# Performance work log

Hardware: AMD Instinct MI355X
Metric: run time of the kernel (lower is better)

Reference implementation:

```python
import jax, jax.numpy as jnp
import numpy as np

D = 1024
H = 16
L = 2048
B = 2
EPS = 1e-5


def setup_inputs() -> dict:
    key = jax.random.key(0)
    ks = jax.random.split(key, 12)
    s = 0.02
    return {
        "x": jax.random.normal(ks[0], (B, L, D), dtype=jnp.float32),
        "ln1_w": jnp.ones((D,), jnp.float32),
        "ln1_b": jnp.zeros((D,), jnp.float32),
        "ln2_w": jnp.ones((D,), jnp.float32),
        "ln2_b": jnp.zeros((D,), jnp.float32),
        "attn_w": jax.random.normal(ks[1], (D, 3 * D), jnp.float32) * s,
        "attn_b": jnp.zeros((3 * D,), jnp.float32),
        "proj_w": jax.random.normal(ks[2], (D, D), jnp.float32) * s,
        "proj_b": jnp.zeros((D,), jnp.float32),
        "fc1_w": jax.random.normal(ks[3], (D, 4 * D), jnp.float32) * s,
        "fc1_b": jnp.zeros((4 * D,), jnp.float32),
        "fc2_w": jax.random.normal(ks[4], (4 * D, D), jnp.float32) * s,
        "fc2_b": jnp.zeros((D,), jnp.float32),
    }


def layernorm(x, w, b):
    mu = jnp.mean(x, axis=-1, keepdims=True)
    var = jnp.mean(jnp.square(x - mu), axis=-1, keepdims=True)
    return (x - mu) * jax.lax.rsqrt(var + EPS) * w + b


def reference(x, ln1_w, ln1_b, ln2_w, ln2_b, attn_w, attn_b,
              proj_w, proj_b, fc1_w, fc1_b, fc2_w, fc2_b):
    Bsz, Lq, C = x.shape
    hd = C // H

    # --- attention branch ---
    h = layernorm(x, ln1_w, ln1_b)
    qkv = h @ attn_w + attn_b                      # [B, L, 3C]
    q, k, v = jnp.split(qkv, 3, axis=-1)
    q = q.reshape(Bsz, Lq, H, hd).transpose(0, 2, 1, 3)  # [B, H, L, hd]
    k = k.reshape(Bsz, Lq, H, hd).transpose(0, 2, 1, 3)
    v = v.reshape(Bsz, Lq, H, hd).transpose(0, 2, 1, 3)

    # NOTE: original scales by 1/sqrt(embedding_dim), not sqrt(head_dim)
    att = jnp.einsum('bhqd,bhkd->bhqk', q, k) / jnp.sqrt(jnp.float32(C))
    causal = jnp.tril(jnp.ones((Lq, Lq), dtype=bool))
    att = jnp.where(causal[None, None], att, jnp.float32(-jnp.inf))
    att = jax.nn.softmax(att, axis=-1)
    y = jnp.einsum('bhqk,bhkd->bhqd', att, v)      # [B, H, L, hd]
    y = y.transpose(0, 2, 1, 3).reshape(Bsz, Lq, C)
    y = y @ proj_w + proj_b
    x = x + y

    # --- MLP branch ---
    h = layernorm(x, ln2_w, ln2_b)
    h = jax.nn.gelu(h @ fc1_w + fc1_b, approximate=False)
    h = h @ fc2_w + fc2_b
    return x + h
```

## Files before the change

kernel.cpp:

```cpp
#include <hip/hip_runtime.h>

#define Bsz 2
#define Lq  2048
#define Dm  1024
#define Hh  16

typedef __attribute__((ext_vector_type(8))) short bf16x8;
typedef __attribute__((ext_vector_type(4))) float f32x4;

#define MFMA16(a, b, c) __builtin_amdgcn_mfma_f32_16x16x32_bf16((a), (b), (c), 0, 0, 0)
#define EXP2F(x) __builtin_amdgcn_exp2f(x)

__device__ __forceinline__ short f2bf(float f) {
    union { float f; unsigned u; } v; v.f = f;
    unsigned r = v.u + 0x7fffu + ((v.u >> 16) & 1u);
    return (short)(r >> 16);
}

__device__ __forceinline__ float bf2f(unsigned short s) {
    union { float f; unsigned u; } t; t.u = ((unsigned)s) << 16;
    return t.f;
}

__device__ __forceinline__ int pk2(float a, float b) {
    union { float f; unsigned u; } ua, ub; ua.f = a; ub.f = b;
    return (int)((ua.u >> 16) | (ub.u & 0xffff0000u));
}

__device__ __forceinline__ void gload16(const void* g, void* l) {
    __builtin_amdgcn_global_load_lds((const __attribute__((address_space(1))) void*)g,
                                     (__attribute__((address_space(3))) void*)l,
                                     16, 0, 0);
}

__global__ __launch_bounds__(256) void ln_bf16(const float* __restrict__ x,
                                               const float* __restrict__ w,
                                               const float* __restrict__ b,
                                               short* __restrict__ out) {
    const int row = blockIdx.x;
    const int tid = threadIdx.x;
    const float4 v = ((const float4*)(x + (size_t)row * 1024))[tid];
    float s = v.x + v.y + v.z + v.w;
    float q = v.x * v.x + v.y * v.y + v.z * v.z + v.w * v.w;
    for (int off = 32; off > 0; off >>= 1) {
        s += __shfl_down(s, off);
        q += __shfl_down(q, off);
    }
    __shared__ float red[8];
    const int wave = tid >> 6;
    if ((tid & 63) == 0) { red[wave] = s; red[wave + 4] = q; }
    __syncthreads();
    s = red[0] + red[1] + red[2] + red[3];
    q = red[4] + red[5] + red[6] + red[7];
    const float mu = s * (1.0f / 1024.0f);
    const float var = q * (1.0f / 1024.0f) - mu * mu;
    const float rstd = rsqrtf(var + 1e-5f);
    const float4 wv = ((const float4*)w)[tid];
    const float4 bv = ((const float4*)b)[tid];
    short4 o;
    o.x = f2bf((v.x - mu) * rstd * wv.x + bv.x);
    o.y = f2bf((v.y - mu) * rstd * wv.y + bv.y);
    o.z = f2bf((v.z - mu) * rstd * wv.z + bv.z);
    o.w = f2bf((v.w - mu) * rstd * wv.w + bv.w);
    ((short4*)(out + (size_t)row * 1024))[tid] = o;
}

__global__ __launch_bounds__(256) void tr_cvt_all(
    const float* __restrict__ attnw, const float* __restrict__ projw,
    const float* __restrict__ fc1w,  const float* __restrict__ fc2w,
    short* __restrict__ attnwT, short* __restrict__ projwT,
    short* __restrict__ fc1wT,  short* __restrict__ fc2wT) {
    int id = blockIdx.x;
    const float* W; short* Wt; int K, N, bx, by;
    if (id < 3072)      { W = attnw; Wt = attnwT; K = 1024; N = 3072; bx = id % 96;  by = id / 96; }
    else if (id < 4096) { id -= 3072; W = projw; Wt = projwT; K = 1024; N = 1024; bx = id & 31; by = id >> 5; }
    else if (id < 8192) { id -= 4096; W = fc1w;  Wt = fc1wT;  K = 1024; N = 4096; bx = id & 127; by = id >> 7; }
    else                { id -= 8192; W = fc2w;  Wt = fc2wT;  K = 4096; N = 1024; bx = id & 31; by = id >> 5; }
    __shared__ float t[32][33];
    const int n0 = bx * 32, k0 = by * 32;
    const int tx = threadIdx.x & 31, ty = threadIdx.x >> 5;
#pragma unroll
    for (int i = 0; i < 4; i++)
        t[ty + i * 8][tx] = W[(size_t)(k0 + ty + i * 8) * N + n0 + tx];
    __syncthreads();
#pragma unroll
    for (int i = 0; i < 4; i++)
        Wt[(size_t)(n0 + ty + i * 8) * K + k0 + tx] = f2bf(t[tx][ty + i * 8]);
}

template <int EP>
__global__ __launch_bounds__(256, 4) void gemm_bt(
    const short* __restrict__ A, const short* __restrict__ Bt,
    const float* __restrict__ bias, int N, int K,
    short* __restrict__ qd, short* __restrict__ kd, short* __restrict__ vtd,
    short* __restrict__ outb) {
    __shared__ short As[128 * 64];
    __shared__ short Bs[128 * 64];
    const int tid = threadIdx.x;
    const int lane = tid & 63, w = tid >> 6;
    const int l16 = lane & 15, quad = lane >> 4;
    const int wr = (w & 1) * 64, wc = (w >> 1) * 64;
    const int n = blockIdx.x;
    const int row0 = ((n & 7) * 4 + ((n >> 3) & 3)) * 128;
    const int col0 = (n >> 5) * 128;
    const int srow = lane >> 3;
    const int scol = ((lane & 7) ^ srow) * 8;

    f32x4 acc[4][4];
    const f32x4 z = {0.f, 0.f, 0.f, 0.f};
#pragma unroll
    for (int i = 0; i < 4; i++)
#pragma unroll
        for (int j = 0; j < 4; j++) acc[i][j] = z;

    const size_t arow = (size_t)(row0 + w * 32 + srow);
    const size_t brow = (size_t)(col0 + w * 32 + srow);

    for (int k0 = 0; k0 < K; k0 += 64) {
#pragma unroll
        for (int g = 0; g < 4; g++) {
            gload16(A + (arow + g * 8) * K + k0 + scol,  &As[(w * 32 + g * 8) * 64]);
            gload16(Bt + (brow + g * 8) * K + k0 + scol, &Bs[(w * 32 + g * 8) * 64]);
        }
        __syncthreads();
#pragma unroll
        for (int kk = 0; kk < 2; kk++) {
            const int rsl = ((kk * 4 + quad) ^ (l16 & 7)) * 8;
            bf16x8 a[4], bb[4];
#pragma unroll
            for (int i = 0; i < 4; i++) a[i] = *(const bf16x8*)&As[(wr + i * 16 + l16) * 64 + rsl];
#pragma unroll
            for (int j = 0; j < 4; j++) bb[j] = *(const bf16x8*)&Bs[(wc + j * 16 + l16) * 64 + rsl];
#pragma unroll
            for (int i = 0; i < 4; i++)
#pragma unroll
                for (int j = 0; j < 4; j++) acc[i][j] = MFMA16(a[i], bb[j], acc[i][j]);
        }
        __syncthreads();
    }

    float bz[4];
#pragma unroll
    for (int j = 0; j < 4; j++) bz[j] = bias[col0 + wc + j * 16 + l16];

#pragma unroll
    for (int i = 0; i < 4; i++) {
#pragma unroll
        for (int r = 0; r < 4; r++) {
            const int grow = row0 + wr + i * 16 + quad * 4 + r;
#pragma unroll
            for (int j = 0; j < 4; j++) {
                const int gcol = col0 + wc + j * 16 + l16;
                const float v = acc[i][j][r] + bz[j];
                if constexpr (EP == 0) {
                    const int b = grow >> 11, l = grow & 2047;
                    const int sec = gcol >> 10, wi = gcol & 1023;
                    const int h = wi >> 6, d = wi & 63;
                    if (sec == 2) {
                        vtd[(((size_t)b * Hh + h) * 64 + d) * Lq + l] = f2bf(v);
                    } else {
                        short* dst = sec ? kd : qd;
                        dst[(((size_t)b * Hh + h) * Lq + l) * 64 + d] = f2bf(v);
                    }
                } else {
                    const float g = 0.5f * v * (1.0f + erff(v * 0.70710678118f));
                    outb[(size_t)grow * N + gcol] = f2bf(g);
                }
            }
        }
    }
}

__global__ __launch_bounds__(256, 4) void gemm_sk(
    const short* __restrict__ A, const short* __restrict__ Bt, int K, int zbits,
    short* __restrict__ Cp) {
    __shared__ short As[128 * 64];
    __shared__ short Bs[128 * 64];
    const int tid = threadIdx.x;
    const int lane = tid & 63, w = tid >> 6;
    const int l16 = lane & 15, quad = lane >> 4;
    const int wr = (w & 1) * 64, wc = (w >> 1) * 64;
    const int n = blockIdx.x;
    const int xcd = n & 7, t = n >> 3;
    const int col = t & 7, u = t >> 3;
    const int c = xcd * (4 << zbits) + u;
    const int zsl = c & ((1 << zbits) - 1);
    const int row0 = (c >> zbits) * 128, col0 = col * 128;
    const int KS = K >> zbits;
    const int kbeg = zsl * KS, kend = kbeg + KS;
    const int srow = lane >> 3;
    const int scol = ((lane & 7) ^ srow) * 8;

    f32x4 acc[4][4];
    const f32x4 z = {0.f, 0.f, 0.f, 0.f};
#pragma unroll
    for (int i = 0; i < 4; i++)
#pragma unroll
        for (int j = 0; j < 4; j++) acc[i][j] = z;

    const size_t arow = (size_t)(row0 + w * 32 + srow);
    const size_t brow = (size_t)(col0 + w * 32 + srow);

    for (int k0 = kbeg; k0 < kend; k0 += 64) {
#pragma unroll
        for (int g = 0; g < 4; g++) {
            gload16(A + (arow + g * 8) * K + k0 + scol,  &As[(w * 32 + g * 8) * 64]);
            gload16(Bt + (brow + g * 8) * K + k0 + scol, &Bs[(w * 32 + g * 8) * 64]);
        }
        __syncthreads();
#pragma unroll
        for (int kk = 0; kk < 2; kk++) {
            const int rsl = ((kk * 4 + quad) ^ (l16 & 7)) * 8;
            bf16x8 a[4], bb[4];
#pragma unroll
            for (int i = 0; i < 4; i++) a[i] = *(const bf16x8*)&As[(wr + i * 16 + l16) * 64 + rsl];
#pragma unroll
            for (int j = 0; j < 4; j++) bb[j] = *(const bf16x8*)&Bs[(wc + j * 16 + l16) * 64 + rsl];
#pragma unroll
            for (int i = 0; i < 4; i++)
#pragma unroll
                for (int j = 0; j < 4; j++) acc[i][j] = MFMA16(a[i], bb[j], acc[i][j]);
        }
        __syncthreads();
    }

    short* cp = Cp + (size_t)zsl * 4096 * 1024;
#pragma unroll
    for (int i = 0; i < 4; i++) {
#pragma unroll
        for (int r = 0; r < 4; r++) {
            const int grow = row0 + wr + i * 16 + quad * 4 + r;
#pragma unroll
            for (int j = 0; j < 4; j++) {
                const int gcol = col0 + wc + j * 16 + l16;
                cp[(size_t)grow * 1024 + gcol] = f2bf(acc[i][j][r]);
            }
        }
    }
}

__global__ __launch_bounds__(256) void sk_reduce(const short* __restrict__ Cp, int S,
                                                 const float* __restrict__ res,
                                                 const float* __restrict__ bias,
                                                 float* __restrict__ out) {
    const int row = blockIdx.x, tid = threadIdx.x;
    const size_t base = (size_t)row * 1024 + tid * 4;
    float4 a = ((const float4*)(res + (size_t)row * 1024))[tid];
    const float4 bz = ((const float4*)bias)[tid];
    a.x += bz.x; a.y += bz.y; a.z += bz.z; a.w += bz.w;
    for (int s = 0; s < S; s++) {
        const ushort4 c = *(const ushort4*)(Cp + (size_t)s * 4096 * 1024 + base);
        a.x += bf2f(c.x); a.y += bf2f(c.y); a.z += bf2f(c.z); a.w += bf2f(c.w);
    }
    *(float4*)(out + base) = a;
}

__global__ __launch_bounds__(256) void sk_reduce_ln(const short* __restrict__ Cp, int S,
                                                    const float* __restrict__ res,
                                                    const float* __restrict__ bias,
                                                    const float* __restrict__ lnw,
                                                    const float* __restrict__ lnb,
                                                    float* __restrict__ xout,
                                                    short* __restrict__ hout) {
    const int row = blockIdx.x, tid = threadIdx.x;
    const size_t base = (size_t)row * 1024 + tid * 4;
    float4 a = ((const float4*)(res + (size_t)row * 1024))[tid];
    const float4 bz = ((const float4*)bias)[tid];
    a.x += bz.x; a.y += bz.y; a.z += bz.z; a.w += bz.w;
    for (int s = 0; s < S; s++) {
        const ushort4 c = *(const ushort4*)(Cp + (size_t)s * 4096 * 1024 + base);
        a.x += bf2f(c.x); a.y += bf2f(c.y); a.z += bf2f(c.z); a.w += bf2f(c.w);
    }
    *(float4*)(xout + base) = a;
    float sm = a.x + a.y + a.z + a.w;
    float qs = a.x * a.x + a.y * a.y + a.z * a.z + a.w * a.w;
    for (int off = 32; off > 0; off >>= 1) {
        sm += __shfl_down(sm, off);
        qs += __shfl_down(qs, off);
    }
    __shared__ float red[8];
    const int wave = tid >> 6;
    if ((tid & 63) == 0) { red[wave] = sm; red[wave + 4] = qs; }
    __syncthreads();
    sm = red[0] + red[1] + red[2] + red[3];
    qs = red[4] + red[5] + red[6] + red[7];
    const float mu = sm * (1.0f / 1024.0f);
    const float var = qs * (1.0f / 1024.0f) - mu * mu;
    const float rstd = rsqrtf(var + 1e-5f);
    const float4 wv = ((const float4*)lnw)[tid];
    const float4 bv = ((const float4*)lnb)[tid];
    short4 o;
    o.x = f2bf((a.x - mu) * rstd * wv.x + bv.x);
    o.y = f2bf((a.y - mu) * rstd * wv.y + bv.y);
    o.z = f2bf((a.z - mu) * rstd * wv.z + bv.z);
    o.w = f2bf((a.w - mu) * rstd * wv.w + bv.w);
    ((short4*)(hout + (size_t)row * 1024))[tid] = o;
}

#define KP 72
__global__ __launch_bounds__(256, 2) void attn_kernel(const short* __restrict__ Q,
                                                      const short* __restrict__ Kb,
                                                      const short* __restrict__ Vt,
                                                      short* __restrict__ Y) {
    const int tid = threadIdx.x;
    const int lane = tid & 63, wave = tid >> 6;
    const int l16 = lane & 15, quad = lane >> 4;
    const int qblk = 15 - blockIdx.x;
    const int bh = blockIdx.y;
    const int qw = qblk * 128 + wave * 32;

    const short* qg = Q + ((size_t)bh * Lq + qw) * 64;
    const short* kg = Kb + (size_t)bh * Lq * 64;
    const short* vg = Vt + (size_t)bh * 64 * Lq;

    __shared__ short sKa[2][64 * 32], sKb[2][64 * 32];
    __shared__ short sVa[2][64 * 32], sVb[2][64 * 32];
    __shared__ short sP[4][32 * KP];
    short* wpP = sP[wave];

    const float c1 = 0.0450842213f;

    bf16x8 qf[2][2];
#pragma unroll
    for (int c = 0; c < 2; c++)
#pragma unroll
        for (int d = 0; d < 2; d++) {
            bf16x8 v = *(const bf16x8*)(qg + (c * 16 + l16) * 64 + d * 32 + quad * 8);
            bf16x8 r;
#pragma unroll
            for (int i = 0; i < 8; i++) {
                union { float f; unsigned u; } t;
                t.u = ((unsigned)(unsigned short)v[i]) << 16;
                r[i] = f2bf(t.f * c1);
            }
            qf[c][d] = r;
        }

    f32x4 o[4][2];
    const f32x4 z = {0.f, 0.f, 0.f, 0.f};
#pragma unroll
    for (int j = 0; j < 4; j++)
#pragma unroll
        for (int c = 0; c < 2; c++) o[j][c] = z;
    float l_i[2] = {0.f, 0.f};

    const int srow = wave * 16 + (lane >> 2);
    const int scol = (lane & 3) * 8;
    const int nst = 2 * qblk + 2;

    auto stage = [&](int s) {
        const int p = s & 1;
        const int kb = s * 64;
        gload16(kg + (size_t)(kb + srow) * 64 + scol,      &sKa[p][(wave * 16) * 32]);
        gload16(kg + (size_t)(kb + srow) * 64 + 32 + scol, &sKb[p][(wave * 16) * 32]);
        gload16(vg + (size_t)srow * Lq + kb + scol,        &sVa[p][(wave * 16) * 32]);
        gload16(vg + (size_t)srow * Lq + kb + 32 + scol,   &sVb[p][(wave * 16) * 32]);
    };

    stage(0);

    for (int s = 0; s < nst; ++s) {
        const int p = s & 1;
        __syncthreads();
        bf16x8 kf[4][2];
#pragma unroll
        for (int kt = 0; kt < 4; kt++) {
            kf[kt][0] = *(const bf16x8*)&sKa[p][(kt * 16 + l16) * 32 + quad * 8];
            kf[kt][1] = *(const bf16x8*)&sKb[p][(kt * 16 + l16) * 32 + quad * 8];
        }
        if (s + 1 < nst) stage(s + 1);

        f32x4 st[4][2];
#pragma unroll
        for (int kt = 0; kt < 4; kt++)
#pragma unroll
            for (int c = 0; c < 2; c++) {
                st[kt][c] = MFMA16(kf[kt][0], qf[c][0], z);
                st[kt][c] = MFMA16(kf[kt][1], qf[c][1], st[kt][c]);
            }

        const int rel = s * 64 - qblk * 128 - wave * 32;
        if (rel > -64) {
#pragma unroll
            for (int kt = 0; kt < 4; kt++)
#pragma unroll
                for (int c = 0; c < 2; c++)
#pragma unroll
                    for (int r = 0; r < 4; r++) {
                        const int krel = rel + kt * 16 + quad * 4 + r - c * 16;
                        if (krel > l16) st[kt][c][r] = -1e30f;
                    }
        }

#pragma unroll
        for (int c = 0; c < 2; c++) {
            float pv[4][4], rs = 0.f;
#pragma unroll
            for (int kt = 0; kt < 4; kt++)
#pragma unroll
                for (int r = 0; r < 4; r++) {
                    pv[kt][r] = EXP2F(st[kt][c][r]);
                    rs += pv[kt][r];
                }
            l_i[c] += rs;
            short* wp = wpP + (c * 16 + l16) * KP;
#pragma unroll
            for (int kt = 0; kt < 4; kt++) {
                int2 pw; pw.x = pk2(pv[kt][0], pv[kt][1]); pw.y = pk2(pv[kt][2], pv[kt][3]);
                *(int2*)(wp + kt * 16 + quad * 4) = pw;
            }
        }

        bf16x8 pf[2][2];
#pragma unroll
        for (int c = 0; c < 2; c++) {
            pf[c][0] = *(const bf16x8*)(wpP + (c * 16 + l16) * KP + quad * 8);
            pf[c][1] = *(const bf16x8*)(wpP + (c * 16 + l16) * KP + 32 + quad * 8);
        }
#pragma unroll
        for (int j = 0; j < 4; j++) {
            const bf16x8 v0 = *(const bf16x8*)&sVa[p][(j * 16 + l16) * 32 + quad * 8];
            const bf16x8 v1 = *(const bf16x8*)&sVb[p][(j * 16 + l16) * 32 + quad * 8];
#pragma unroll
            for (int c = 0; c < 2; c++) {
                o[j][c] = MFMA16(v0, pf[c][0], o[j][c]);
                o[j][c] = MFMA16(v1, pf[c][1], o[j][c]);
            }
        }
    }

    const int b = bh >> 4, h = bh & 15;
#pragma unroll
    for (int c = 0; c < 2; c++) {
        float ls = l_i[c];
        ls += __shfl_xor(ls, 16);
        ls += __shfl_xor(ls, 32);
        const float inv = 1.0f / ls;
        const size_t base = ((size_t)b * Lq + qw + c * 16 + l16) * 1024 + h * 64;
#pragma unroll
        for (int j = 0; j < 4; j++) {
            short4 s4;
            s4.x = f2bf(o[j][c][0] * inv);
            s4.y = f2bf(o[j][c][1] * inv);
            s4.z = f2bf(o[j][c][2] * inv);
            s4.w = f2bf(o[j][c][3] * inv);
            *(short4*)(Y + base + j * 16 + quad * 4) = s4;
        }
    }
}

extern "C" void kernel_launch(void* const* d_in, const int* in_sizes, int n_in,
                              void* d_out, int out_size, void* d_ws, size_t ws_size,
                              hipStream_t stream) {
    (void)in_sizes; (void)n_in; (void)out_size; (void)ws_size;
    const float* x     = (const float*)d_in[0];
    const float* ln1w  = (const float*)d_in[1];
    const float* ln1b  = (const float*)d_in[2];
    const float* ln2w  = (const float*)d_in[3];
    const float* ln2b  = (const float*)d_in[4];
    const float* attnw = (const float*)d_in[5];
    const float* attnb = (const float*)d_in[6];
    const float* projw = (const float*)d_in[7];
    const float* projb = (const float*)d_in[8];
    const float* fc1w  = (const float*)d_in[9];
    const float* fc1b  = (const float*)d_in[10];
    const float* fc2w  = (const float*)d_in[11];
    const float* fc2b  = (const float*)d_in[12];
    float* out = (float*)d_out;

    char* ws = (char*)d_ws;
    size_t off = 0;
    auto alloc = [&](size_t bytes) {
        void* p = ws + off;
        off += (bytes + 255) & ~(size_t)255;
        return p;
    };
    short* attnwT = (short*)alloc(3072ull * 1024 * 2);
    short* projwT = (short*)alloc(1024ull * 1024 * 2);
    short* fc1wT  = (short*)alloc(4096ull * 1024 * 2);
    short* fc2wT  = (short*)alloc(1024ull * 4096 * 2);
    short* hbuf   = (short*)alloc(4096ull * 1024 * 2);
    short* qbuf   = (short*)alloc(4096ull * 1024 * 2);
    short* kbuf   = (short*)alloc(4096ull * 1024 * 2);
    short* vtbuf  = (short*)alloc(4096ull * 1024 * 2);
    short* ybuf   = (short*)alloc(4096ull * 1024 * 2);
    float* x1     = (float*)alloc(4096ull * 1024 * 4);
    short* Cp     = (short*)alloc(4ull * 4096 * 1024 * 2);
    short* hh = qbuf;

    tr_cvt_all<<<12288, 256, 0, stream>>>(attnw, projw, fc1w, fc2w,
                                          attnwT, projwT, fc1wT, fc2wT);

    ln_bf16<<<4096, 256, 0, stream>>>(x, ln1w, ln1b, hbuf);
    gemm_bt<0><<<768, 256, 0, stream>>>(hbuf, attnwT, attnb, 3072, 1024,
                                        qbuf, kbuf, vtbuf, nullptr);
    attn_kernel<<<dim3(16, 32), 256, 0, stream>>>(qbuf, kbuf, vtbuf, ybuf);
    gemm_sk<<<512, 256, 0, stream>>>(ybuf, projwT, 1024, 1, Cp);
    sk_reduce_ln<<<4096, 256, 0, stream>>>(Cp, 2, x, projb, ln2w, ln2b, x1, hbuf);

    gemm_bt<2><<<1024, 256, 0, stream>>>(hbuf, fc1wT, fc1b, 4096, 1024,
                                         nullptr, nullptr, nullptr, hh);
    gemm_sk<<<1024, 256, 0, stream>>>(hh, fc2wT, 4096, 2, Cp);
    sk_reduce<<<4096, 256, 0, stream>>>(Cp, 4, x1, fc2b, out);
}
```

Baseline: 340.6 us.

## Swizzle K/V shared-memory tiles and remap attention blocks across XCDs

K and V tiles move from split half-width LDS buffers to full 64-wide rows with an XOR swizzle on the 16-byte slots. This is meant to cut LDS bank conflicts on the fragment reads and give fuller global load rows. The grid becomes 1D with a mapping that places the four heads of each group on the same XCD (for L2 reuse of K/V) and reverses the q-block order for half the blocks to balance causal work. The risk is that the swizzle indexing must match exactly between the stores and the reads.

```diff
diff --git a/kernel.cpp b/kernel.cpp
--- a/kernel.cpp
+++ b/kernel.cpp
@@ -305,16 +305,19 @@
     const int tid = threadIdx.x;
     const int lane = tid & 63, wave = tid >> 6;
     const int l16 = lane & 15, quad = lane >> 4;
-    const int qblk = 15 - blockIdx.x;
-    const int bh = blockIdx.y;
+    const int n = blockIdx.x;
+    const int xcd = n & 7, m = n >> 3;
+    const int bh = xcd * 4 + (m & 3);
+    const int mm = (m & 31) >> 2;
+    const int qblk = (m < 32) ? (15 - mm) : mm;
     const int qw = qblk * 128 + wave * 32;
 
     const short* qg = Q + ((size_t)bh * Lq + qw) * 64;
     const short* kg = Kb + (size_t)bh * Lq * 64;
     const short* vg = Vt + (size_t)bh * 64 * Lq;
 
-    __shared__ short sKa[2][64 * 32], sKb[2][64 * 32];
-    __shared__ short sVa[2][64 * 32], sVb[2][64 * 32];
+    __shared__ short sK[2][64 * 64];
+    __shared__ short sV[2][64 * 64];
     __shared__ short sP[4][32 * KP];
     short* wpP = sP[wave];
 
@@ -344,17 +347,18 @@
         for (int c = 0; c < 2; c++) o[j][c] = z;
     float l_i[2] = {0.f, 0.f};
 
-    const int srow = wave * 16 + (lane >> 2);
-    const int scol = (lane & 3) * 8;
+    const int srow8 = lane >> 3;
+    const int sslot = ((lane & 7) ^ srow8) * 8;
+    const int r0 = wave * 16;
     const int nst = 2 * qblk + 2;
 
     auto stage = [&](int s) {
         const int p = s & 1;
         const int kb = s * 64;
-        gload16(kg + (size_t)(kb + srow) * 64 + scol,      &sKa[p][(wave * 16) * 32]);
-        gload16(kg + (size_t)(kb + srow) * 64 + 32 + scol, &sKb[p][(wave * 16) * 32]);
-        gload16(vg + (size_t)srow * Lq + kb + scol,        &sVa[p][(wave * 16) * 32]);
-        gload16(vg + (size_t)srow * Lq + kb + 32 + scol,   &sVb[p][(wave * 16) * 32]);
+        gload16(kg + (size_t)(kb + r0 + srow8) * 64 + sslot,     &sK[p][r0 * 64]);
+        gload16(kg + (size_t)(kb + r0 + 8 + srow8) * 64 + sslot, &sK[p][(r0 + 8) * 64]);
+        gload16(vg + (size_t)(r0 + srow8) * Lq + kb + sslot,     &sV[p][r0 * 64]);
+        gload16(vg + (size_t)(r0 + 8 + srow8) * Lq + kb + sslot, &sV[p][(r0 + 8) * 64]);
     };
 
     stage(0);
@@ -364,10 +368,11 @@
         __syncthreads();
         bf16x8 kf[4][2];
 #pragma unroll
-        for (int kt = 0; kt < 4; kt++) {
-            kf[kt][0] = *(const bf16x8*)&sKa[p][(kt * 16 + l16) * 32 + quad * 8];
-            kf[kt][1] = *(const bf16x8*)&sKb[p][(kt * 16 + l16) * 32 + quad * 8];
-        }
+        for (int kt = 0; kt < 4; kt++)
+#pragma unroll
+            for (int d = 0; d < 2; d++)
+                kf[kt][d] = *(const bf16x8*)&sK[p][(kt * 16 + l16) * 64 +
+                                                   (((d * 4 + quad) ^ (l16 & 7)) * 8)];
         if (s + 1 < nst) stage(s + 1);
 
         f32x4 st[4][2];
@@ -419,8 +424,10 @@
         }
 #pragma unroll
         for (int j = 0; j < 4; j++) {
-            const bf16x8 v0 = *(const bf16x8*)&sVa[p][(j * 16 + l16) * 32 + quad * 8];
-            const bf16x8 v1 = *(const bf16x8*)&sVb[p][(j * 16 + l16) * 32 + quad * 8];
+            const bf16x8 v0 = *(const bf16x8*)&sV[p][(j * 16 + l16) * 64 +
+                                                     ((quad ^ (l16 & 7)) * 8)];
+            const bf16x8 v1 = *(const bf16x8*)&sV[p][(j * 16 + l16) * 64 +
+                                                     (((4 + quad) ^ (l16 & 7)) * 8)];
 #pragma unroll
             for (int c = 0; c < 2; c++) {
                 o[j][c] = MFMA16(v0, pf[c][0], o[j][c]);
@@ -494,7 +501,7 @@
     ln_bf16<<<4096, 256, 0, stream>>>(x, ln1w, ln1b, hbuf);
     gemm_bt<0><<<768, 256, 0, stream>>>(hbuf, attnwT, attnb, 3072, 1024,
                                         qbuf, kbuf, vtbuf, nullptr);
-    attn_kernel<<<dim3(16, 32), 256, 0, stream>>>(qbuf, kbuf, vtbuf, ybuf);
+    attn_kernel<<<512, 256, 0, stream>>>(qbuf, kbuf, vtbuf, ybuf);
     gemm_sk<<<512, 256, 0, stream>>>(ybuf, projwT, 1024, 1, Cp);
     sk_reduce_ln<<<4096, 256, 0, stream>>>(Cp, 2, x, projb, ln2w, ln2b, x1, hbuf);
 
```

Result: faster. 325.3 us (-4.5%).
